# Optimization experiments

Hardware: AMD Instinct MI355X
Metric: run time of the kernel (lower is better)

## Reference

```python
import jax, jax.numpy as jnp
from jax import lax
import numpy as np

DN = ('NCDHW', 'OIDHW', 'NCDHW')


def _conv3(x, w, b):
    # standard 3x3x3 conv, stride 1, pad 1
    y = lax.conv_general_dilated(x, w, (1, 1, 1), ((1, 1), (1, 1), (1, 1)), dimension_numbers=DN)
    return y + b[None, :, None, None, None]


def _bn(x, gamma, beta, eps=1e-5):
    # training-mode batchnorm over (N, D, H, W), biased variance (torch semantics)
    mean = jnp.mean(x, axis=(0, 2, 3, 4), keepdims=True)
    var = jnp.var(x, axis=(0, 2, 3, 4), keepdims=True)
    return gamma[None, :, None, None, None] * (x - mean) * lax.rsqrt(var + eps) + beta[None, :, None, None, None]


def _deform_conv(x, off, w):
    # ConvOffset3d: one scalar offset per deformable group shifting the temporal (D)
    # sampling position of every kernel tap; linear interpolation along D, zero padding.
    N, C, D, H, W = x.shape
    G = off.shape[1]
    cpg = C // G
    offc = jnp.repeat(off, cpg, axis=1)                        # [N,C,D,H,W]
    base = offc + jnp.arange(D, dtype=x.dtype)[None, None, :, None, None]
    out = None
    for kd in range(3):                                        # 3 temporal taps
        pos = base + (kd - 1)                                  # fractional sample pos along D
        f0 = jnp.floor(pos)
        frac = pos - f0
        i0 = f0.astype(jnp.int32)
        i1 = i0 + 1
        m0 = ((i0 >= 0) & (i0 < D)).astype(x.dtype)
        m1 = ((i1 >= 0) & (i1 < D)).astype(x.dtype)
        g = (jnp.take_along_axis(x, jnp.clip(i0, 0, D - 1), axis=2) * ((1.0 - frac) * m0)
             + jnp.take_along_axis(x, jnp.clip(i1, 0, D - 1), axis=2) * (frac * m1))
        # the D-shift for tap kd is already baked into g -> conv with kernel (1,3,3)
        y = lax.conv_general_dilated(g, w[:, :, kd:kd + 1], (1, 1, 1), ((0, 0), (1, 1), (1, 1)), dimension_numbers=DN)
        out = y if out is None else out + y
    return out


def setup_inputs() -> dict:
    key = jax.random.key(0)
    ks = jax.random.split(key, 4)
    C, cpg = 64, 8
    N, D, H, W = 8, 16, 56, 56
    G = C // cpg
    s = 1.0 / np.sqrt(C * 27).astype(np.float32)
    x = jax.random.normal(ks[0], (N, C, D, H, W), jnp.float32)
    w_off = jax.random.normal(ks[1], (G, C, 3, 3, 3), jnp.float32) * s
    b_off = jnp.zeros((G,), jnp.float32)
    w1 = jax.random.normal(ks[2], (C, C, 3, 3, 3), jnp.float32) * s
    w2 = jax.random.normal(ks[3], (C, C, 3, 3, 3), jnp.float32) * s
    b2 = jnp.zeros((C,), jnp.float32)
    return dict(x=x, w_off=w_off, b_off=b_off, w1=w1, w2=w2, b2=b2,
                bn1_gamma=jnp.ones((C,), jnp.float32), bn1_beta=jnp.zeros((C,), jnp.float32),
                bn2_gamma=jnp.ones((C,), jnp.float32), bn2_beta=jnp.zeros((C,), jnp.float32))


def reference(x, w_off, b_off, w1, w2, b2, bn1_gamma, bn1_beta, bn2_gamma, bn2_beta):
    off = _conv3(x, w_off, b_off)               # [N, G, D, H, W]
    out = _deform_conv(x, off, w1)              # deformable conv (no bias)
    out = jax.nn.relu(_bn(out, bn1_gamma, bn1_beta))
    out = _conv3(out, w2, b2)
    out = _bn(out, bn2_gamma, bn2_beta) + x     # residual
    out = jax.nn.relu(out)
    return (out, off)
```

## Files before the change

kernel.cpp:

```cpp
#include <hip/hip_runtime.h>

#define HW 3136
#define DHW 50176
#define NEL 25690112
#define CNT 401408.0f

typedef __attribute__((ext_vector_type(8)))  short          short8;
typedef __attribute__((ext_vector_type(8)))  unsigned short ushort8;
typedef __attribute__((ext_vector_type(4)))  float          f32x4;
typedef __attribute__((ext_vector_type(16))) float          f32x16;

__device__ __forceinline__ unsigned f2bf(float f) {
    union { float f; unsigned u; } v; v.f = f;
    return (v.u + 0x7FFFu + ((v.u >> 16) & 1u)) >> 16;
}
__device__ __forceinline__ float bf2f(unsigned u) {
    union { unsigned u; float f; } v; v.u = u << 16;
    return v.f;
}
__device__ __forceinline__ unsigned cvt_pk_bf16(float lo, float hi) {
    unsigned r;
    asm("v_cvt_pk_bf16_f32 %0, %1, %2" : "=v"(r) : "v"(lo), "v"(hi));
    return r;
}

__device__ __forceinline__ void xcd_decode(int& h, int& d, int& n, int& bucket) {
    const int bid = blockIdx.x + 56 * (blockIdx.y + 16 * blockIdx.z);
    bucket = bid & 63;
    const int swz = (bid & 7) * 896 + (bid >> 3);
    h = swz % 56;
    const int dn = swz / 56;
    d = dn & 15;
    n = dn >> 4;
}

__global__ __launch_bounds__(256) void k_transpose(
    const float* __restrict__ x, unsigned short* __restrict__ xt)
{
    __shared__ unsigned lds[4][64 * 36];
    const int d = blockIdx.x, n = blockIdx.y, z = blockIdx.z;
    const int wave = threadIdx.x >> 6, lane = threadIdx.x & 63;
    const float* xb = x + (size_t)n * 64 * DHW + d * HW;
    unsigned short* xtb = xt + (size_t)n * DHW * 64;
    unsigned* L = lds[wave];

    for (int c = z * 7 + wave; c < z * 7 + 7 && c < 49; c += 4) {
        const int P = c * 64;
#pragma unroll 4
        for (int cp = 0; cp < 32; ++cp) {
            const float a = xb[(size_t)(2 * cp) * DHW + P + lane];
            const float b = xb[(size_t)(2 * cp + 1) * DHW + P + lane];
            L[lane * 36 + cp] = cvt_pk_bf16(a, b);
        }
#pragma unroll
        for (int k = 0; k < 8; ++k) {
            const int r = (lane >> 3) + 8 * k;
            const uint4 v = *(const uint4*)&L[r * 36 + 4 * (lane & 7)];
            *(uint4*)((char*)xtb + ((size_t)(P + r) * 16 + d) * 128 + (lane & 7) * 16) = v;
        }
    }
}

__global__ __launch_bounds__(256) void k_wprep(
    const float* __restrict__ w_off, const float* __restrict__ w1,
    const float* __restrict__ w2, unsigned short* __restrict__ BtO,
    unsigned short* __restrict__ Bt1, unsigned short* __restrict__ Bt2)
{
    const int i = blockIdx.x * 256 + threadIdx.x;
    if (i < 27648) {
        const int tap = i / 1024, r = i - tap * 1024;
        const int ks = r >> 9, r3 = r & 511, lane = r3 >> 3, e = r3 & 7;
        const int row = lane & 15;
        const int ci  = ks * 32 + (lane >> 4) * 8 + e;
        BtO[i] = (row < 8) ? (unsigned short)f2bf(w_off[(row * 64 + ci) * 27 + tap]) : 0;
    }
    if (i < 110592) {
        const int tap = i / 4096, r = i - tap * 4096;
        const int cog = r >> 11, r2 = r & 2047;
        const int ksw = r2 >> 10, r3 = r2 & 1023;
        const int ksub = r3 >> 9, r4 = r3 & 511;
        const int lane = r4 >> 3, e = r4 & 7;
        const int co = cog * 32 + (lane & 31);
        const int ci = ksw * 32 + ksub * 16 + (lane >> 5) * 8 + e;
        Bt1[i] = (unsigned short)f2bf(w1[(co * 64 + ci) * 27 + tap]);
        Bt2[i] = (unsigned short)f2bf(w2[(co * 64 + ci) * 27 + tap]);
    }
}

template<int NCO, bool BN, bool DIN>
__global__ __launch_bounds__(512) void k_conv(
    const unsigned short* __restrict__ src, const unsigned short* __restrict__ Bt,
    const float* __restrict__ bias, const float* __restrict__ scv,
    const float* __restrict__ shv, float* __restrict__ dst,
    float* __restrict__ osum, float* __restrict__ osq)
{
    __shared__ unsigned short A[538 * 72];
    int h, d, n, bucket;
    xcd_decode(h, d, n, bucket);
    const int tid = threadIdx.x;
    const int wave = tid >> 6, lane = tid & 63, lm = lane & 15, quad = lane >> 4;
    const int k8 = tid & 7;

    float scr[8], shr[8];
    if constexpr (BN) {
#pragma unroll
        for (int e = 0; e < 8; ++e) { scr[e] = scv[k8 * 8 + e]; shr[e] = shv[k8 * 8 + e]; }
    }

    const unsigned short* snb = DIN ? (src + (size_t)n * DHW * 64)
                                    : (src + (size_t)(n * 16) * HW * 64);

    const int spx = tid >> 3;
    const int wq  = spx - 1;
    const bool pxok = (tid < 464) & ((unsigned)wq < 56u);
#pragma unroll
    for (int row = 0; row < 9; ++row) {
        const int kd = row / 3, kh = row - (row / 3) * 3;
        const int dq = d + kd - 1, hq = h + kh - 1;
        uint4 pk = {0u, 0u, 0u, 0u};
        if (pxok & ((unsigned)dq < 16u) & ((unsigned)hq < 56u)) {
            const size_t off = DIN ? (((size_t)(hq * 56 + wq) * 16 + dq) * 64)
                                   : (((size_t)dq * HW + hq * 56 + wq) * 64);
            const ushort8 val = *(const ushort8*)(snb + off + k8 * 8);
            if constexpr (BN) {
                float f[8];
#pragma unroll
                for (int e = 0; e < 8; ++e)
                    f[e] = fmaxf(fmaf(bf2f(val[e]), scr[e], shr[e]), 0.f);
                pk.x = cvt_pk_bf16(f[0], f[1]);
                pk.y = cvt_pk_bf16(f[2], f[3]);
                pk.z = cvt_pk_bf16(f[4], f[5]);
                pk.w = cvt_pk_bf16(f[6], f[7]);
            } else {
                pk = *(const uint4*)&val;
            }
        }
        if (tid < 464) *(uint4*)&A[(size_t)(row * 58 + spx) * 72 + k8 * 8] = pk;
    }
    __syncthreads();

    if constexpr (NCO == 8) {
        const int ksw = wave >> 2, mf = wave & 3;
        f32x4 acc = (f32x4){0.f, 0.f, 0.f, 0.f};
        const unsigned short* Btb = Bt + ksw * 512;
        unsigned boff = (unsigned)lane * 8;
        short8 bc = *(const short8*)(Btb + boff);
        boff += 1024u;
        unsigned arow = (unsigned)(mf * 16 + lm) * 72 + quad * 8 + ksw * 32;
#pragma unroll 1
        for (int r9 = 0; r9 < 9; ++r9) {
#pragma unroll
            for (int kw = 0; kw < 3; ++kw) {
                const bool more = (kw < 2) | (r9 < 8);
                short8 bn;
                if (more) bn = *(const short8*)(Btb + boff);
                const short8 a = *(const short8*)&A[arow + kw * 72];
                acc = __builtin_amdgcn_mfma_f32_16x16x32_bf16(a, bc, acc, 0, 0, 0);
                if (more) { bc = bn; boff += 1024u; }
            }
            arow += 58 * 72;
        }
        __syncthreads();
        float* E = (float*)A;
#pragma unroll
        for (int r = 0; r < 4; ++r) {
            const int mm = mf * 16 + quad * 4 + r;
            if (mm < 56) E[ksw * 952 + mm * 17 + lm] = acc[r];
        }
        __syncthreads();
        if (lane < 56) {
            const float v = E[lane * 17 + wave] + E[952 + lane * 17 + wave] + bias[wave];
            dst[((size_t)(n * 8 + wave) * 16 + d) * HW + h * 56 + lane] = v;
        }
    } else {
        const int pxg = wave & 1, cog = (wave >> 1) & 1, ksw = wave >> 2;
        f32x16 acc = (f32x16){0.f,0.f,0.f,0.f,0.f,0.f,0.f,0.f,
                              0.f,0.f,0.f,0.f,0.f,0.f,0.f,0.f};

        const unsigned short* Btb = Bt + (unsigned)(cog * 2 + ksw) * 1024;
        unsigned boff = (unsigned)lane * 8;
        short8 bc0 = *(const short8*)(Btb + boff);
        short8 bc1 = *(const short8*)(Btb + boff + 512);
        boff += 4096u;
        unsigned arow = (unsigned)(pxg * 32 + (lane & 31)) * 72 + ksw * 32 + (lane >> 5) * 8;

#pragma unroll 1
        for (int r9 = 0; r9 < 9; ++r9) {
#pragma unroll
            for (int kw = 0; kw < 3; ++kw) {
                const bool more = (kw < 2) | (r9 < 8);
                short8 bn0, bn1;
                if (more) {
                    bn0 = *(const short8*)(Btb + boff);
                    bn1 = *(const short8*)(Btb + boff + 512);
                }
                const unsigned ab = arow + kw * 72;
                const short8 a0 = *(const short8*)&A[ab];
                const short8 a1 = *(const short8*)&A[ab + 16];
                acc = __builtin_amdgcn_mfma_f32_32x32x16_bf16(a0, bc0, acc, 0, 0, 0);
                acc = __builtin_amdgcn_mfma_f32_32x32x16_bf16(a1, bc1, acc, 0, 0, 0);
                if (more) { bc0 = bn0; bc1 = bn1; boff += 4096u; }
            }
            arow += 58 * 72;
        }

        __syncthreads();
        float* E = (float*)A;
#pragma unroll
        for (int reg = 0; reg < 16; ++reg) {
            const int pl = (reg & 3) + 8 * (reg >> 2) + 4 * (lane >> 5);
            E[ksw * 4160 + (pxg * 32 + pl) * 65 + cog * 32 + (lane & 31)] = acc[reg];
        }
        __syncthreads();
        const int co = tid >> 3, w8 = tid & 7;
        const float bco = bias[co];
        float* drow = &dst[((size_t)(n * 64 + co) * 16 + d) * HW + h * 56];
        float s = 0.f, q = 0.f;
#pragma unroll
        for (int i = 0; i < 7; ++i) {
            const int w0 = w8 + 8 * i;
            const float v = E[w0 * 65 + co] + E[4160 + w0 * 65 + co] + bco;
            drow[w0] = v;
            s += v; q = fmaf(v, v, q);
        }
        s += __shfl_down(s, 1); q += __shfl_down(q, 1);
        s += __shfl_down(s, 2); q += __shfl_down(q, 2);
        s += __shfl_down(s, 4); q += __shfl_down(q, 4);
        if ((lane & 7) == 0) {
            atomicAdd(&osum[(bucket << 6) + co], s);
            atomicAdd(&osq [(bucket << 6) + co], q);
        }
    }
}

__global__ __launch_bounds__(512) void k_deform(
    const unsigned short* __restrict__ xt, const float* __restrict__ offo,
    const unsigned short* __restrict__ Bt, unsigned short* __restrict__ out1,
    float* __restrict__ osum, float* __restrict__ osq)
{
    __shared__ unsigned short A[538 * 72];
    int h, d, n, bucket;
    xcd_decode(h, d, n, bucket);
    const int tid = threadIdx.x;
    const int wave = tid >> 6, lane = tid & 63;

    float pv[3];
#pragma unroll
    for (int it = 0; it < 3; ++it) {
        const int c = tid + it * 512;
        float p = 0.f;
        if (c < 1392) {
            const int g = c & 7, pix = c >> 3;
            const int hq3 = pix / 58, px = pix - hq3 * 58;
            const int habs = h + hq3 - 1, wq = px - 1;
            if (((unsigned)habs < 56u) & ((unsigned)wq < 56u))
                p = offo[((size_t)(n * 8 + g) * 16 + d) * HW + habs * 56 + wq] + (float)d;
        }
        pv[it] = p;
    }

#pragma unroll
    for (int it = 0; it < 3; ++it) {
        const int c = tid + it * 512;
        if (c >= 1392) break;
        const int g = c & 7, pix = c >> 3;
        const int hq3 = pix / 58, px = pix - hq3 * 58;
        const int habs = h + hq3 - 1, wq = px - 1;
        uint4 p0 = {0u,0u,0u,0u}, p1 = {0u,0u,0u,0u}, p2 = {0u,0u,0u,0u};
        if (((unsigned)habs < 56u) & ((unsigned)wq < 56u)) {
            const float p = pv[it];
            const float fl = floorf(p);
            const float fr = p - fl;
            const int i0 = (int)fl;
            const unsigned short* cb = xt + ((size_t)n * HW + habs * 56 + wq) * (16 * 64) + g * 8;
            float sv[4][8], m[4];
#pragma unroll
            for (int j = 0; j < 4; ++j) {
                const int dj = i0 - 1 + j;
                const bool ok = (unsigned)dj < 16u;
                m[j] = ok ? 1.f : 0.f;
                const ushort8 v = *(const ushort8*)(cb + (size_t)(ok ? dj : 0) * 64);
#pragma unroll
                for (int e = 0; e < 8; ++e) sv[j][e] = bf2f(v[e]);
            }
            const float fi = 1.f - fr;
            const float w0a = fi * m[0], w0b = fr * m[1];
            const float w1a = fi * m[1], w1b = fr * m[2];
            const float w2a = fi * m[2], w2b = fr * m[3];
            float a0[8], a1[8], a2[8];
#pragma unroll
            for (int e = 0; e < 8; ++e) {
                a0[e] = fmaf(sv[1][e], w0b, sv[0][e] * w0a);
                a1[e] = fmaf(sv[2][e], w1b, sv[1][e] * w1a);
                a2[e] = fmaf(sv[3][e], w2b, sv[2][e] * w2a);
            }
            p0.x = cvt_pk_bf16(a0[0], a0[1]); p0.y = cvt_pk_bf16(a0[2], a0[3]);
            p0.z = cvt_pk_bf16(a0[4], a0[5]); p0.w = cvt_pk_bf16(a0[6], a0[7]);
            p1.x = cvt_pk_bf16(a1[0], a1[1]); p1.y = cvt_pk_bf16(a1[2], a1[3]);
            p1.z = cvt_pk_bf16(a1[4], a1[5]); p1.w = cvt_pk_bf16(a1[6], a1[7]);
            p2.x = cvt_pk_bf16(a2[0], a2[1]); p2.y = cvt_pk_bf16(a2[2], a2[3]);
            p2.z = cvt_pk_bf16(a2[4], a2[5]); p2.w = cvt_pk_bf16(a2[6], a2[7]);
        }
        const int sl = hq3 * 58 + px;
        *(uint4*)&A[(size_t)(sl          ) * 72 + g * 8] = p0;
        *(uint4*)&A[(size_t)(sl + 3 * 58 ) * 72 + g * 8] = p1;
        *(uint4*)&A[(size_t)(sl + 6 * 58 ) * 72 + g * 8] = p2;
    }
    __syncthreads();

    const int pxg = wave & 1, cog = (wave >> 1) & 1, ksw = wave >> 2;
    f32x16 acc = (f32x16){0.f,0.f,0.f,0.f,0.f,0.f,0.f,0.f,
                          0.f,0.f,0.f,0.f,0.f,0.f,0.f,0.f};

    const unsigned short* Btb = Bt + (unsigned)(cog * 2 + ksw) * 1024;
    unsigned boff = (unsigned)lane * 8;
    short8 bc0 = *(const short8*)(Btb + boff);
    short8 bc1 = *(const short8*)(Btb + boff + 512);
    boff += 4096u;
    unsigned arow = (unsigned)(pxg * 32 + (lane & 31)) * 72 + ksw * 32 + (lane >> 5) * 8;

#pragma unroll 1
    for (int r9 = 0; r9 < 9; ++r9) {
#pragma unroll
        for (int kw = 0; kw < 3; ++kw) {
            const bool more = (kw < 2) | (r9 < 8);
            short8 bn0, bn1;
            if (more) {
                bn0 = *(const short8*)(Btb + boff);
                bn1 = *(const short8*)(Btb + boff + 512);
            }
            const unsigned ab = arow + kw * 72;
            const short8 a0 = *(const short8*)&A[ab];
            const short8 a1 = *(const short8*)&A[ab + 16];
            acc = __builtin_amdgcn_mfma_f32_32x32x16_bf16(a0, bc0, acc, 0, 0, 0);
            acc = __builtin_amdgcn_mfma_f32_32x32x16_bf16(a1, bc1, acc, 0, 0, 0);
            if (more) { bc0 = bn0; bc1 = bn1; boff += 4096u; }
        }
        arow += 58 * 72;
    }

    __syncthreads();
    float* E = (float*)A;
#pragma unroll
    for (int reg = 0; reg < 16; ++reg) {
        const int pl = (reg & 3) + 8 * (reg >> 2) + 4 * (lane >> 5);
        E[ksw * 4160 + (pxg * 32 + pl) * 65 + cog * 32 + (lane & 31)] = acc[reg];
    }
    __syncthreads();
    const size_t pixb = ((size_t)(n * 16) + d) * HW + h * 56;
    if (tid < 448) {
        const int px = tid >> 3, kk = tid & 7;
        float v[8];
#pragma unroll
        for (int e = 0; e < 8; ++e)
            v[e] = E[px * 65 + kk * 8 + e] + E[4160 + px * 65 + kk * 8 + e];
        uint4 pk;
        pk.x = cvt_pk_bf16(v[0], v[1]); pk.y = cvt_pk_bf16(v[2], v[3]);
        pk.z = cvt_pk_bf16(v[4], v[5]); pk.w = cvt_pk_bf16(v[6], v[7]);
        *(uint4*)(out1 + (pixb + px) * 64 + kk * 8) = pk;
    }
    const int co = tid >> 3, w8 = tid & 7;
    float s = 0.f, q = 0.f;
#pragma unroll
    for (int i = 0; i < 7; ++i) {
        const int w0 = w8 + 8 * i;
        const float v = E[w0 * 65 + co] + E[4160 + w0 * 65 + co];
        s += v; q = fmaf(v, v, q);
    }
    s += __shfl_down(s, 1); q += __shfl_down(q, 1);
    s += __shfl_down(s, 2); q += __shfl_down(q, 2);
    s += __shfl_down(s, 4); q += __shfl_down(q, 4);
    if ((lane & 7) == 0) {
        atomicAdd(&osum[(bucket << 6) + co], s);
        atomicAdd(&osq [(bucket << 6) + co], q);
    }
}

__global__ void k_finalize(const float* __restrict__ sums, const float* __restrict__ sqs,
                           const float* __restrict__ gamma, const float* __restrict__ beta,
                           float* __restrict__ scale, float* __restrict__ shift)
{
    const int c = threadIdx.x;
    float s = 0.f, q = 0.f;
#pragma unroll 8
    for (int b = 0; b < 64; ++b) {
        s += sums[(b << 6) + c];
        q += sqs [(b << 6) + c];
    }
    const float mean = s / CNT;
    const float var  = q / CNT - mean * mean;
    const float sc   = gamma[c] * rsqrtf(var + 1e-5f);
    scale[c] = sc;
    shift[c] = fmaf(-mean, sc, beta[c]);
}

__global__ __launch_bounds__(256) void k_residual(
    float4* __restrict__ dst, const float4* __restrict__ raw,
    const float4* __restrict__ x,
    const float* __restrict__ scale, const float* __restrict__ shift)
{
    const int i = blockIdx.x * 256 + threadIdx.x;
    const int c = (i / 12544) & 63;
    const float sc = scale[c], sh = shift[c];
    float4 v = raw[i];
    const float4 xv = x[i];
    v.x = fmaxf(fmaf(v.x, sc, sh) + xv.x, 0.f);
    v.y = fmaxf(fmaf(v.y, sc, sh) + xv.y, 0.f);
    v.z = fmaxf(fmaf(v.z, sc, sh) + xv.z, 0.f);
    v.w = fmaxf(fmaf(v.w, sc, sh) + xv.w, 0.f);
    dst[i] = v;
}

extern "C" void kernel_launch(void* const* d_in, const int* in_sizes, int n_in,
                              void* d_out, int out_size, void* d_ws, size_t ws_size,
                              hipStream_t stream) {
    const float* x     = (const float*)d_in[0];
    const float* w_off = (const float*)d_in[1];
    const float* b_off = (const float*)d_in[2];
    const float* w1    = (const float*)d_in[3];
    const float* w2    = (const float*)d_in[4];
    const float* b2    = (const float*)d_in[5];
    const float* g1    = (const float*)d_in[6];
    const float* be1   = (const float*)d_in[7];
    const float* g2    = (const float*)d_in[8];
    const float* be2   = (const float*)d_in[9];

    float* out     = (float*)d_out;
    float* off_out = out + NEL;
    unsigned short* out1 = (unsigned short*)d_out;
    unsigned short* wb   = (unsigned short*)(out + 13000000);
    unsigned short* BtO  = wb;
    unsigned short* Bt1  = BtO + 27648;
    unsigned short* Bt2  = Bt1 + 110592;

    unsigned short* xt  = (unsigned short*)d_ws;
    float*          raw = (float*)d_ws;

    float* stb = (float*)((char*)d_out + 53000000);
    float* dsum = stb,        * dsq = stb + 4096;
    float* csum = stb + 8192, * csq = stb + 12288;
    float* shp = (float*)d_ws + NEL;
    float* sc1 = shp,       * sh1 = shp + 64;
    float* sc2 = shp + 128, * sh2 = shp + 192;

    hipMemsetAsync(stb, 0, 16384 * sizeof(float), stream);

    k_transpose<<<dim3(16, 8, 7), 256, 0, stream>>>(x, xt);
    k_wprep<<<432, 256, 0, stream>>>(w_off, w1, w2, BtO, Bt1, Bt2);

    const dim3 cgrid(56, 16, 8);
    k_conv<8, false, true><<<cgrid, 512, 0, stream>>>(xt, BtO, b_off, nullptr, nullptr, off_out, nullptr, nullptr);
    k_deform<<<cgrid, 512, 0, stream>>>(xt, off_out, Bt1, out1, dsum, dsq);

    k_finalize<<<1, 64, 0, stream>>>(dsum, dsq, g1, be1, sc1, sh1);

    k_conv<64, true, false><<<cgrid, 512, 0, stream>>>(out1, Bt2, b2, sc1, sh1, raw, csum, csq);

    k_finalize<<<1, 64, 0, stream>>>(csum, csq, g2, be2, sc2, sh2);
    k_residual<<<25088, 256, 0, stream>>>((float4*)out, (const float4*)raw, (const float4*)x, sc2, sh2);
}
```

Measured before the change: 663.2 us.

## Process two output rows per block in deform and 64-channel conv kernels

The deformable conv and the second 3x3x3 conv now compute two adjacent H rows per block with 1024 threads, staging a 4-row halo (12 rows instead of 9 per output row) in LDS. This cuts redundant halo loads and the D-interpolation work per output row, and halves the block count. The cost is a larger LDS footprint, 1024-thread blocks that may lower occupancy, and a serialized two-pass epilogue for the two rows. The template kernel is split into separate k_conv8 and k_conv64 kernels.

Measured after the change: 686.2 us. 3.5% more time.

```diff
diff --git a/kernel.cpp b/kernel.cpp
--- a/kernel.cpp
+++ b/kernel.cpp
@@ -24,12 +24,20 @@
     return r;
 }
 
-__device__ __forceinline__ void xcd_decode(int& h, int& d, int& n, int& bucket) {
+__device__ __forceinline__ void xcd_decode(int& h, int& d, int& n) {
     const int bid = blockIdx.x + 56 * (blockIdx.y + 16 * blockIdx.z);
-    bucket = bid & 63;
     const int swz = (bid & 7) * 896 + (bid >> 3);
     h = swz % 56;
     const int dn = swz / 56;
+    d = dn & 15;
+    n = dn >> 4;
+}
+__device__ __forceinline__ void xcd_decode28(int& hblk, int& d, int& n, int& bucket) {
+    const int bid = blockIdx.x + 28 * (blockIdx.y + 16 * blockIdx.z);
+    bucket = bid & 63;
+    const int swz = (bid & 7) * 448 + (bid >> 3);
+    hblk = swz % 28;
+    const int dn = swz / 28;
     d = dn & 15;
     n = dn >> 4;
 }
@@ -87,28 +95,18 @@
     }
 }
 
-template<int NCO, bool BN, bool DIN>
-__global__ __launch_bounds__(512) void k_conv(
+__global__ __launch_bounds__(512) void k_conv8(
     const unsigned short* __restrict__ src, const unsigned short* __restrict__ Bt,
-    const float* __restrict__ bias, const float* __restrict__ scv,
-    const float* __restrict__ shv, float* __restrict__ dst,
-    float* __restrict__ osum, float* __restrict__ osq)
+    const float* __restrict__ bias, float* __restrict__ dst)
 {
     __shared__ unsigned short A[538 * 72];
-    int h, d, n, bucket;
-    xcd_decode(h, d, n, bucket);
+    int h, d, n;
+    xcd_decode(h, d, n);
     const int tid = threadIdx.x;
     const int wave = tid >> 6, lane = tid & 63, lm = lane & 15, quad = lane >> 4;
     const int k8 = tid & 7;
 
-    float scr[8], shr[8];
-    if constexpr (BN) {
-#pragma unroll
-        for (int e = 0; e < 8; ++e) { scr[e] = scv[k8 * 8 + e]; shr[e] = shv[k8 * 8 + e]; }
-    }
-
-    const unsigned short* snb = DIN ? (src + (size_t)n * DHW * 64)
-                                    : (src + (size_t)(n * 16) * HW * 64);
+    const unsigned short* snb = src + (size_t)n * DHW * 64;
 
     const int spx = tid >> 3;
     const int wq  = spx - 1;
@@ -119,140 +117,183 @@
         const int dq = d + kd - 1, hq = h + kh - 1;
         uint4 pk = {0u, 0u, 0u, 0u};
         if (pxok & ((unsigned)dq < 16u) & ((unsigned)hq < 56u)) {
-            const size_t off = DIN ? (((size_t)(hq * 56 + wq) * 16 + dq) * 64)
-                                   : (((size_t)dq * HW + hq * 56 + wq) * 64);
+            const size_t off = ((size_t)(hq * 56 + wq) * 16 + dq) * 64;
+            pk = *(const uint4*)(snb + off + k8 * 8);
+        }
+        if (tid < 464) *(uint4*)&A[(size_t)(row * 58 + spx) * 72 + k8 * 8] = pk;
+    }
+    __syncthreads();
+
+    const int ksw = wave >> 2, mf = wave & 3;
+    f32x4 acc = (f32x4){0.f, 0.f, 0.f, 0.f};
+    const unsigned short* Btb = Bt + ksw * 512;
+    unsigned boff = (unsigned)lane * 8;
+    short8 bc = *(const short8*)(Btb + boff);
+    boff += 1024u;
+    unsigned arow = (unsigned)(mf * 16 + lm) * 72 + quad * 8 + ksw * 32;
+#pragma unroll 1
+    for (int r9 = 0; r9 < 9; ++r9) {
+#pragma unroll
+        for (int kw = 0; kw < 3; ++kw) {
+            const bool more = (kw < 2) | (r9 < 8);
+            short8 bn;
+            if (more) bn = *(const short8*)(Btb + boff);
+            const short8 a = *(const short8*)&A[arow + kw * 72];
+            acc = __builtin_amdgcn_mfma_f32_16x16x32_bf16(a, bc, acc, 0, 0, 0);
+            if (more) { bc = bn; boff += 1024u; }
+        }
+        arow += 58 * 72;
+    }
+    __syncthreads();
+    float* E = (float*)A;
+#pragma unroll
+    for (int r = 0; r < 4; ++r) {
+        const int mm = mf * 16 + quad * 4 + r;
+        if (mm < 56) E[ksw * 952 + mm * 17 + lm] = acc[r];
+    }
+    __syncthreads();
+    if (lane < 56) {
+        const float v = E[lane * 17 + wave] + E[952 + lane * 17 + wave] + bias[wave];
+        dst[((size_t)(n * 8 + wave) * 16 + d) * HW + h * 56 + lane] = v;
+    }
+}
+
+__global__ __launch_bounds__(1024) void k_conv64(
+    const unsigned short* __restrict__ src, const unsigned short* __restrict__ Bt,
+    const float* __restrict__ bias, const float* __restrict__ scv,
+    const float* __restrict__ shv, float* __restrict__ dst,
+    float* __restrict__ osum, float* __restrict__ osq)
+{
+    __shared__ unsigned short A[712 * 72];
+    int hblk, d, n, bucket;
+    xcd_decode28(hblk, d, n, bucket);
+    const int h0 = hblk * 2;
+    const int tid = threadIdx.x;
+    const int wave = tid >> 6, lane = tid & 63;
+    const int k8 = tid & 7;
+
+    float scr[8], shr[8];
+#pragma unroll
+    for (int e = 0; e < 8; ++e) { scr[e] = scv[k8 * 8 + e]; shr[e] = shv[k8 * 8 + e]; }
+
+    const unsigned short* snb = src + (size_t)(n * 16) * HW * 64;
+
+    const int sub = tid & 511, rr = tid >> 9;
+    const int spx = sub >> 3;
+    const int wq  = spx - 1;
+    const bool pxok = (sub < 464) & ((unsigned)wq < 56u);
+#pragma unroll
+    for (int i = 0; i < 6; ++i) {
+        const int row = i * 2 + rr;
+        const int kd = row >> 2, hqi = row & 3;
+        const int dq = d + kd - 1, hq = h0 + hqi - 1;
+        uint4 pk = {0u, 0u, 0u, 0u};
+        if (pxok & ((unsigned)dq < 16u) & ((unsigned)hq < 56u)) {
+            const size_t off = ((size_t)dq * HW + hq * 56 + wq) * 64;
             const ushort8 val = *(const ushort8*)(snb + off + k8 * 8);
-            if constexpr (BN) {
-                float f[8];
-#pragma unroll
-                for (int e = 0; e < 8; ++e)
-                    f[e] = fmaxf(fmaf(bf2f(val[e]), scr[e], shr[e]), 0.f);
-                pk.x = cvt_pk_bf16(f[0], f[1]);
-                pk.y = cvt_pk_bf16(f[2], f[3]);
-                pk.z = cvt_pk_bf16(f[4], f[5]);
-                pk.w = cvt_pk_bf16(f[6], f[7]);
-            } else {
-                pk = *(const uint4*)&val;
-            }
-        }
-        if (tid < 464) *(uint4*)&A[(size_t)(row * 58 + spx) * 72 + k8 * 8] = pk;
+            float f[8];
+#pragma unroll
+            for (int e = 0; e < 8; ++e)
+                f[e] = fmaxf(fmaf(bf2f(val[e]), scr[e], shr[e]), 0.f);
+            pk.x = cvt_pk_bf16(f[0], f[1]);
+            pk.y = cvt_pk_bf16(f[2], f[3]);
+            pk.z = cvt_pk_bf16(f[4], f[5]);
+            pk.w = cvt_pk_bf16(f[6], f[7]);
+        }
+        if (sub < 464) *(uint4*)&A[(size_t)(row * 58 + spx) * 72 + k8 * 8] = pk;
     }
     __syncthreads();
 
-    if constexpr (NCO == 8) {
-        const int ksw = wave >> 2, mf = wave & 3;
-        f32x4 acc = (f32x4){0.f, 0.f, 0.f, 0.f};
-        const unsigned short* Btb = Bt + ksw * 512;
-        unsigned boff = (unsigned)lane * 8;
-        short8 bc = *(const short8*)(Btb + boff);
-        boff += 1024u;
-        unsigned arow = (unsigned)(mf * 16 + lm) * 72 + quad * 8 + ksw * 32;
+    const int hs = wave & 1, pxg = (wave >> 1) & 1, cog = (wave >> 2) & 1, ksw = wave >> 3;
+    f32x16 acc = (f32x16){0.f,0.f,0.f,0.f,0.f,0.f,0.f,0.f,
+                          0.f,0.f,0.f,0.f,0.f,0.f,0.f,0.f};
+    const unsigned short* Btb = Bt + (unsigned)(cog * 2 + ksw) * 1024;
+    unsigned boff = (unsigned)lane * 8;
+    short8 bc0 = *(const short8*)(Btb + boff);
+    short8 bc1 = *(const short8*)(Btb + boff + 512);
+    boff += 4096u;
+    const unsigned arow = (unsigned)(hs * 58 + pxg * 32 + (lane & 31)) * 72
+                        + ksw * 32 + (lane >> 5) * 8;
+
 #pragma unroll 1
-        for (int r9 = 0; r9 < 9; ++r9) {
+    for (int kd = 0; kd < 3; ++kd) {
+#pragma unroll
+        for (int kh = 0; kh < 3; ++kh) {
 #pragma unroll
             for (int kw = 0; kw < 3; ++kw) {
-                const bool more = (kw < 2) | (r9 < 8);
-                short8 bn;
-                if (more) bn = *(const short8*)(Btb + boff);
-                const short8 a = *(const short8*)&A[arow + kw * 72];
-                acc = __builtin_amdgcn_mfma_f32_16x16x32_bf16(a, bc, acc, 0, 0, 0);
-                if (more) { bc = bn; boff += 1024u; }
-            }
-            arow += 58 * 72;
-        }
-        __syncthreads();
-        float* E = (float*)A;
-#pragma unroll
-        for (int r = 0; r < 4; ++r) {
-            const int mm = mf * 16 + quad * 4 + r;
-            if (mm < 56) E[ksw * 952 + mm * 17 + lm] = acc[r];
-        }
-        __syncthreads();
-        if (lane < 56) {
-            const float v = E[lane * 17 + wave] + E[952 + lane * 17 + wave] + bias[wave];
-            dst[((size_t)(n * 8 + wave) * 16 + d) * HW + h * 56 + lane] = v;
-        }
-    } else {
-        const int pxg = wave & 1, cog = (wave >> 1) & 1, ksw = wave >> 2;
-        f32x16 acc = (f32x16){0.f,0.f,0.f,0.f,0.f,0.f,0.f,0.f,
-                              0.f,0.f,0.f,0.f,0.f,0.f,0.f,0.f};
-
-        const unsigned short* Btb = Bt + (unsigned)(cog * 2 + ksw) * 1024;
-        unsigned boff = (unsigned)lane * 8;
-        short8 bc0 = *(const short8*)(Btb + boff);
-        short8 bc1 = *(const short8*)(Btb + boff + 512);
-        boff += 4096u;
-        unsigned arow = (unsigned)(pxg * 32 + (lane & 31)) * 72 + ksw * 32 + (lane >> 5) * 8;
-
-#pragma unroll 1
-        for (int r9 = 0; r9 < 9; ++r9) {
-#pragma unroll
-            for (int kw = 0; kw < 3; ++kw) {
-                const bool more = (kw < 2) | (r9 < 8);
+                const bool more = !((kd == 2) & (kh == 2) & (kw == 2));
                 short8 bn0, bn1;
                 if (more) {
                     bn0 = *(const short8*)(Btb + boff);
                     bn1 = *(const short8*)(Btb + boff + 512);
                 }
-                const unsigned ab = arow + kw * 72;
+                const unsigned ab = arow + (unsigned)(((kd * 4 + kh) * 58 + kw) * 72);
                 const short8 a0 = *(const short8*)&A[ab];
                 const short8 a1 = *(const short8*)&A[ab + 16];
                 acc = __builtin_amdgcn_mfma_f32_32x32x16_bf16(a0, bc0, acc, 0, 0, 0);
                 acc = __builtin_amdgcn_mfma_f32_32x32x16_bf16(a1, bc1, acc, 0, 0, 0);
                 if (more) { bc0 = bn0; bc1 = bn1; boff += 4096u; }
             }
-            arow += 58 * 72;
-        }
-
+        }
+    }
+
+    float* E = (float*)A;
+#pragma unroll 1
+    for (int hss = 0; hss < 2; ++hss) {
         __syncthreads();
-        float* E = (float*)A;
-#pragma unroll
-        for (int reg = 0; reg < 16; ++reg) {
-            const int pl = (reg & 3) + 8 * (reg >> 2) + 4 * (lane >> 5);
-            E[ksw * 4160 + (pxg * 32 + pl) * 65 + cog * 32 + (lane & 31)] = acc[reg];
+        if (hs == hss) {
+#pragma unroll
+            for (int reg = 0; reg < 16; ++reg) {
+                const int pl = (reg & 3) + 8 * (reg >> 2) + 4 * (lane >> 5);
+                E[ksw * 4160 + (pxg * 32 + pl) * 65 + cog * 32 + (lane & 31)] = acc[reg];
+            }
         }
         __syncthreads();
-        const int co = tid >> 3, w8 = tid & 7;
+        const int co = tid >> 4, w16 = tid & 15;
         const float bco = bias[co];
-        float* drow = &dst[((size_t)(n * 64 + co) * 16 + d) * HW + h * 56];
+        float* drow = &dst[((size_t)(n * 64 + co) * 16 + d) * HW + (h0 + hss) * 56];
         float s = 0.f, q = 0.f;
 #pragma unroll
-        for (int i = 0; i < 7; ++i) {
-            const int w0 = w8 + 8 * i;
-            const float v = E[w0 * 65 + co] + E[4160 + w0 * 65 + co] + bco;
-            drow[w0] = v;
-            s += v; q = fmaf(v, v, q);
+        for (int i = 0; i < 4; ++i) {
+            const int w0 = w16 + 16 * i;
+            if (w0 < 56) {
+                const float v = E[w0 * 65 + co] + E[4160 + w0 * 65 + co] + bco;
+                drow[w0] = v;
+                s += v; q = fmaf(v, v, q);
+            }
         }
         s += __shfl_down(s, 1); q += __shfl_down(q, 1);
         s += __shfl_down(s, 2); q += __shfl_down(q, 2);
         s += __shfl_down(s, 4); q += __shfl_down(q, 4);
-        if ((lane & 7) == 0) {
+        s += __shfl_down(s, 8); q += __shfl_down(q, 8);
+        if ((lane & 15) == 0) {
             atomicAdd(&osum[(bucket << 6) + co], s);
             atomicAdd(&osq [(bucket << 6) + co], q);
         }
     }
 }
 
-__global__ __launch_bounds__(512) void k_deform(
+__global__ __launch_bounds__(1024) void k_deform(
     const unsigned short* __restrict__ xt, const float* __restrict__ offo,
     const unsigned short* __restrict__ Bt, unsigned short* __restrict__ out1,
     float* __restrict__ osum, float* __restrict__ osq)
 {
-    __shared__ unsigned short A[538 * 72];
-    int h, d, n, bucket;
-    xcd_decode(h, d, n, bucket);
+    __shared__ unsigned short A[712 * 72];
+    int hblk, d, n, bucket;
+    xcd_decode28(hblk, d, n, bucket);
+    const int h0 = hblk * 2;
     const int tid = threadIdx.x;
     const int wave = tid >> 6, lane = tid & 63;
 
-    float pv[3];
-#pragma unroll
-    for (int it = 0; it < 3; ++it) {
-        const int c = tid + it * 512;
+    float pv[2];
+#pragma unroll
+    for (int it = 0; it < 2; ++it) {
+        const int c = tid + it * 1024;
         float p = 0.f;
-        if (c < 1392) {
+        if (c < 1856) {
             const int g = c & 7, pix = c >> 3;
-            const int hq3 = pix / 58, px = pix - hq3 * 58;
-            const int habs = h + hq3 - 1, wq = px - 1;
+            const int hqi = pix / 58, px = pix - hqi * 58;
+            const int habs = h0 + hqi - 1, wq = px - 1;
             if (((unsigned)habs < 56u) & ((unsigned)wq < 56u))
                 p = offo[((size_t)(n * 8 + g) * 16 + d) * HW + habs * 56 + wq] + (float)d;
         }
@@ -260,119 +301,130 @@
     }
 
 #pragma unroll
-    for (int it = 0; it < 3; ++it) {
-        const int c = tid + it * 512;
-        if (c >= 1392) break;
-        const int g = c & 7, pix = c >> 3;
-        const int hq3 = pix / 58, px = pix - hq3 * 58;
-        const int habs = h + hq3 - 1, wq = px - 1;
-        uint4 p0 = {0u,0u,0u,0u}, p1 = {0u,0u,0u,0u}, p2 = {0u,0u,0u,0u};
-        if (((unsigned)habs < 56u) & ((unsigned)wq < 56u)) {
-            const float p = pv[it];
-            const float fl = floorf(p);
-            const float fr = p - fl;
-            const int i0 = (int)fl;
-            const unsigned short* cb = xt + ((size_t)n * HW + habs * 56 + wq) * (16 * 64) + g * 8;
-            float sv[4][8], m[4];
-#pragma unroll
-            for (int j = 0; j < 4; ++j) {
-                const int dj = i0 - 1 + j;
-                const bool ok = (unsigned)dj < 16u;
-                m[j] = ok ? 1.f : 0.f;
-                const ushort8 v = *(const ushort8*)(cb + (size_t)(ok ? dj : 0) * 64);
-#pragma unroll
-                for (int e = 0; e < 8; ++e) sv[j][e] = bf2f(v[e]);
-            }
-            const float fi = 1.f - fr;
-            const float w0a = fi * m[0], w0b = fr * m[1];
-            const float w1a = fi * m[1], w1b = fr * m[2];
-            const float w2a = fi * m[2], w2b = fr * m[3];
-            float a0[8], a1[8], a2[8];
-#pragma unroll
-            for (int e = 0; e < 8; ++e) {
-                a0[e] = fmaf(sv[1][e], w0b, sv[0][e] * w0a);
-                a1[e] = fmaf(sv[2][e], w1b, sv[1][e] * w1a);
-                a2[e] = fmaf(sv[3][e], w2b, sv[2][e] * w2a);
-            }
-            p0.x = cvt_pk_bf16(a0[0], a0[1]); p0.y = cvt_pk_bf16(a0[2], a0[3]);
-            p0.z = cvt_pk_bf16(a0[4], a0[5]); p0.w = cvt_pk_bf16(a0[6], a0[7]);
-            p1.x = cvt_pk_bf16(a1[0], a1[1]); p1.y = cvt_pk_bf16(a1[2], a1[3]);
-            p1.z = cvt_pk_bf16(a1[4], a1[5]); p1.w = cvt_pk_bf16(a1[6], a1[7]);
-            p2.x = cvt_pk_bf16(a2[0], a2[1]); p2.y = cvt_pk_bf16(a2[2], a2[3]);
-            p2.z = cvt_pk_bf16(a2[4], a2[5]); p2.w = cvt_pk_bf16(a2[6], a2[7]);
-        }
-        const int sl = hq3 * 58 + px;
-        *(uint4*)&A[(size_t)(sl          ) * 72 + g * 8] = p0;
-        *(uint4*)&A[(size_t)(sl + 3 * 58 ) * 72 + g * 8] = p1;
-        *(uint4*)&A[(size_t)(sl + 6 * 58 ) * 72 + g * 8] = p2;
+    for (int it = 0; it < 2; ++it) {
+        const int c = tid + it * 1024;
+        if (c < 1856) {
+            const int g = c & 7, pix = c >> 3;
+            const int hqi = pix / 58, px = pix - hqi * 58;
+            const int habs = h0 + hqi - 1, wq = px - 1;
+            uint4 p0 = {0u,0u,0u,0u}, p1 = {0u,0u,0u,0u}, p2 = {0u,0u,0u,0u};
+            if (((unsigned)habs < 56u) & ((unsigned)wq < 56u)) {
+                const float p = pv[it];
+                const float fl = floorf(p);
+                const float fr = p - fl;
+                const int i0 = (int)fl;
+                const unsigned short* cb = xt + ((size_t)n * HW + habs * 56 + wq) * (16 * 64) + g * 8;
+                float sv[4][8], m[4];
+#pragma unroll
+                for (int j = 0; j < 4; ++j) {
+                    const int dj = i0 - 1 + j;
+                    const bool ok = (unsigned)dj < 16u;
+                    m[j] = ok ? 1.f : 0.f;
+                    const ushort8 v = *(const ushort8*)(cb + (size_t)(ok ? dj : 0) * 64);
+#pragma unroll
+                    for (int e = 0; e < 8; ++e) sv[j][e] = bf2f(v[e]);
+                }
+                const float fi = 1.f - fr;
+                const float w0a = fi * m[0], w0b = fr * m[1];
+                const float w1a = fi * m[1], w1b = fr * m[2];
+                const float w2a = fi * m[2], w2b = fr * m[3];
+                float a0[8], a1[8], a2[8];
+#pragma unroll
+                for (int e = 0; e < 8; ++e) {
+                    a0[e] = fmaf(sv[1][e], w0b, sv[0][e] * w0a);
+                    a1[e] = fmaf(sv[2][e], w1b, sv[1][e] * w1a);
+                    a2[e] = fmaf(sv[3][e], w2b, sv[2][e] * w2a);
+                }
+                p0.x = cvt_pk_bf16(a0[0], a0[1]); p0.y = cvt_pk_bf16(a0[2], a0[3]);
+                p0.z = cvt_pk_bf16(a0[4], a0[5]); p0.w = cvt_pk_bf16(a0[6], a0[7]);
+                p1.x = cvt_pk_bf16(a1[0], a1[1]); p1.y = cvt_pk_bf16(a1[2], a1[3]);
+                p1.z = cvt_pk_bf16(a1[4], a1[5]); p1.w = cvt_pk_bf16(a1[6], a1[7]);
+                p2.x = cvt_pk_bf16(a2[0], a2[1]); p2.y = cvt_pk_bf16(a2[2], a2[3]);
+                p2.z = cvt_pk_bf16(a2[4], a2[5]); p2.w = cvt_pk_bf16(a2[6], a2[7]);
+            }
+            const int sl = hqi * 58 + px;
+            *(uint4*)&A[(size_t)(sl           ) * 72 + g * 8] = p0;
+            *(uint4*)&A[(size_t)(sl + 4 * 58  ) * 72 + g * 8] = p1;
+            *(uint4*)&A[(size_t)(sl + 8 * 58  ) * 72 + g * 8] = p2;
+        }
     }
     __syncthreads();
 
-    const int pxg = wave & 1, cog = (wave >> 1) & 1, ksw = wave >> 2;
+    const int hs = wave & 1, pxg = (wave >> 1) & 1, cog = (wave >> 2) & 1, ksw = wave >> 3;
     f32x16 acc = (f32x16){0.f,0.f,0.f,0.f,0.f,0.f,0.f,0.f,
                           0.f,0.f,0.f,0.f,0.f,0.f,0.f,0.f};
-
     const unsigned short* Btb = Bt + (unsigned)(cog * 2 + ksw) * 1024;
     unsigned boff = (unsigned)lane * 8;
     short8 bc0 = *(const short8*)(Btb + boff);
     short8 bc1 = *(const short8*)(Btb + boff + 512);
     boff += 4096u;
-    unsigned arow = (unsigned)(pxg * 32 + (lane & 31)) * 72 + ksw * 32 + (lane >> 5) * 8;
+    const unsigned arow = (unsigned)(hs * 58 + pxg * 32 + (lane & 31)) * 72
+                        + ksw * 32 + (lane >> 5) * 8;
 
 #pragma unroll 1
-    for (int r9 = 0; r9 < 9; ++r9) {
-#pragma unroll
-        for (int kw = 0; kw < 3; ++kw) {
-            const bool more = (kw < 2) | (r9 < 8);
-            short8 bn0, bn1;
-            if (more) {
-                bn0 = *(const short8*)(Btb + boff);
-                bn1 = *(const short8*)(Btb + boff + 512);
-            }
-            const unsigned ab = arow + kw * 72;
-            const short8 a0 = *(const short8*)&A[ab];
-            const short8 a1 = *(const short8*)&A[ab + 16];
-            acc = __builtin_amdgcn_mfma_f32_32x32x16_bf16(a0, bc0, acc, 0, 0, 0);
-            acc = __builtin_amdgcn_mfma_f32_32x32x16_bf16(a1, bc1, acc, 0, 0, 0);
-            if (more) { bc0 = bn0; bc1 = bn1; boff += 4096u; }
-        }
-        arow += 58 * 72;
-    }
-
-    __syncthreads();
+    for (int kd = 0; kd < 3; ++kd) {
+#pragma unroll
+        for (int kh = 0; kh < 3; ++kh) {
+#pragma unroll
+            for (int kw = 0; kw < 3; ++kw) {
+                const bool more = !((kd == 2) & (kh == 2) & (kw == 2));
+                short8 bn0, bn1;
+                if (more) {
+                    bn0 = *(const short8*)(Btb + boff);
+                    bn1 = *(const short8*)(Btb + boff + 512);
+                }
+                const unsigned ab = arow + (unsigned)(((kd * 4 + kh) * 58 + kw) * 72);
+                const short8 a0 = *(const short8*)&A[ab];
+                const short8 a1 = *(const short8*)&A[ab + 16];
+                acc = __builtin_amdgcn_mfma_f32_32x32x16_bf16(a0, bc0, acc, 0, 0, 0);
+                acc = __builtin_amdgcn_mfma_f32_32x32x16_bf16(a1, bc1, acc, 0, 0, 0);
+                if (more) { bc0 = bn0; bc1 = bn1; boff += 4096u; }
+            }
+        }
+    }
+
     float* E = (float*)A;
-#pragma unroll
-    for (int reg = 0; reg < 16; ++reg) {
-        const int pl = (reg & 3) + 8 * (reg >> 2) + 4 * (lane >> 5);
-        E[ksw * 4160 + (pxg * 32 + pl) * 65 + cog * 32 + (lane & 31)] = acc[reg];
-    }
-    __syncthreads();
-    const size_t pixb = ((size_t)(n * 16) + d) * HW + h * 56;
-    if (tid < 448) {
-        const int px = tid >> 3, kk = tid & 7;
-        float v[8];
-#pragma unroll
-        for (int e = 0; e < 8; ++e)
-            v[e] = E[px * 65 + kk * 8 + e] + E[4160 + px * 65 + kk * 8 + e];
-        uint4 pk;
-        pk.x = cvt_pk_bf16(v[0], v[1]); pk.y = cvt_pk_bf16(v[2], v[3]);
-        pk.z = cvt_pk_bf16(v[4], v[5]); pk.w = cvt_pk_bf16(v[6], v[7]);
-        *(uint4*)(out1 + (pixb + px) * 64 + kk * 8) = pk;
-    }
-    const int co = tid >> 3, w8 = tid & 7;
-    float s = 0.f, q = 0.f;
-#pragma unroll
-    for (int i = 0; i < 7; ++i) {
-        const int w0 = w8 + 8 * i;
-        const float v = E[w0 * 65 + co] + E[4160 + w0 * 65 + co];
-        s += v; q = fmaf(v, v, q);
-    }
-    s += __shfl_down(s, 1); q += __shfl_down(q, 1);
-    s += __shfl_down(s, 2); q += __shfl_down(q, 2);
-    s += __shfl_down(s, 4); q += __shfl_down(q, 4);
-    if ((lane & 7) == 0) {
-        atomicAdd(&osum[(bucket << 6) + co], s);
-        atomicAdd(&osq [(bucket << 6) + co], q);
+#pragma unroll 1
+    for (int hss = 0; hss < 2; ++hss) {
+        __syncthreads();
+        if (hs == hss) {
+#pragma unroll
+            for (int reg = 0; reg < 16; ++reg) {
+                const int pl = (reg & 3) + 8 * (reg >> 2) + 4 * (lane >> 5);
+                E[ksw * 4160 + (pxg * 32 + pl) * 65 + cog * 32 + (lane & 31)] = acc[reg];
+            }
+        }
+        __syncthreads();
+        const size_t pixb = ((size_t)(n * 16) + d) * HW + (h0 + hss) * 56;
+        if (tid < 448) {
+            const int px = tid >> 3, kk = tid & 7;
+            float v[8];
+#pragma unroll
+            for (int e = 0; e < 8; ++e)
+                v[e] = E[px * 65 + kk * 8 + e] + E[4160 + px * 65 + kk * 8 + e];
+            uint4 pk;
+            pk.x = cvt_pk_bf16(v[0], v[1]); pk.y = cvt_pk_bf16(v[2], v[3]);
+            pk.z = cvt_pk_bf16(v[4], v[5]); pk.w = cvt_pk_bf16(v[6], v[7]);
+            *(uint4*)(out1 + (pixb + px) * 64 + kk * 8) = pk;
+        }
+        const int co = tid >> 4, w16 = tid & 15;
+        float s = 0.f, q = 0.f;
+#pragma unroll
+        for (int i = 0; i < 4; ++i) {
+            const int w0 = w16 + 16 * i;
+            if (w0 < 56) {
+                const float v = E[w0 * 65 + co] + E[4160 + w0 * 65 + co];
+                s += v; q = fmaf(v, v, q);
+            }
+        }
+        s += __shfl_down(s, 1); q += __shfl_down(q, 1);
+        s += __shfl_down(s, 2); q += __shfl_down(q, 2);
+        s += __shfl_down(s, 4); q += __shfl_down(q, 4);
+        s += __shfl_down(s, 8); q += __shfl_down(q, 8);
+        if ((lane & 15) == 0) {
+            atomicAdd(&osum[(bucket << 6) + co], s);
+            atomicAdd(&osq [(bucket << 6) + co], q);
+        }
     }
 }
 
@@ -448,13 +500,15 @@
     k_transpose<<<dim3(16, 8, 7), 256, 0, stream>>>(x, xt);
     k_wprep<<<432, 256, 0, stream>>>(w_off, w1, w2, BtO, Bt1, Bt2);
 
-    const dim3 cgrid(56, 16, 8);
-    k_conv<8, false, true><<<cgrid, 512, 0, stream>>>(xt, BtO, b_off, nullptr, nullptr, off_out, nullptr, nullptr);
-    k_deform<<<cgrid, 512, 0, stream>>>(xt, off_out, Bt1, out1, dsum, dsq);
+    const dim3 cgrid8(56, 16, 8);
+    const dim3 cgrid2(28, 16, 8);
+
+    k_conv8<<<cgrid8, 512, 0, stream>>>(xt, BtO, b_off, off_out);
+    k_deform<<<cgrid2, 1024, 0, stream>>>(xt, off_out, Bt1, out1, dsum, dsq);
 
     k_finalize<<<1, 64, 0, stream>>>(dsum, dsq, g1, be1, sc1, sh1);
 
-    k_conv<64, true, false><<<cgrid, 512, 0, stream>>>(out1, Bt2, b2, sc1, sh1, raw, csum, csq);
+    k_conv64<<<cgrid2, 1024, 0, stream>>>(out1, Bt2, b2, sc1, sh1, raw, csum, csq);
 
     k_finalize<<<1, 64, 0, stream>>>(csum, csq, g2, be2, sc2, sh2);
     k_residual<<<25088, 256, 0, stream>>>((float4*)out, (const float4*)raw, (const float4*)x, sc2, sh2);
```
